# Optimization experiments

Measured on AMD Instinct MI355X. Metric: run time of the kernel, lower is better.

Reference implementation:

```python
import jax, jax.numpy as jnp
import numpy as np

B, S, IN_DIM, EMBED, HEADS, WINDOW = 2, 2048, 1024, 1024, 16, 256
HEAD_DIM = EMBED // HEADS
NEG_FILL = -9.0e15


def setup_inputs() -> dict:
    key = jax.random.key(0)
    k1, k2, k3, k4 = jax.random.split(key, 4)
    x = jax.random.normal(k1, (B, S, IN_DIM), dtype=jnp.float32)
    # padding_mask: positions with value 1 get zeroed in q/k/v (matches masked_fill semantics)
    padding_mask = jax.random.randint(k2, (B, S), 0, 2, dtype=jnp.int32)
    # xavier-uniform-like init scale for the linear weights
    lim_qkv = np.sqrt(6.0 / (IN_DIM + 3 * EMBED)).astype(np.float32)
    lim_o = np.sqrt(6.0 / (EMBED + EMBED)).astype(np.float32)
    Wqkv = jax.random.uniform(k3, (3 * EMBED, IN_DIM), jnp.float32, -lim_qkv, lim_qkv)
    bqkv = jnp.zeros((3 * EMBED,), jnp.float32)
    Wo = jax.random.uniform(k4, (EMBED, EMBED), jnp.float32, -lim_o, lim_o)
    bo = jnp.zeros((EMBED,), jnp.float32)
    return {"x": x, "padding_mask": padding_mask, "Wqkv": Wqkv, "bqkv": bqkv, "Wo": Wo, "bo": bo}


def reference(x, padding_mask, Wqkv, bqkv, Wo, bo):
    b, s, _ = x.shape
    h, hd, pad = HEADS, HEAD_DIM, WINDOW // 2
    # qkv projection: torch Linear is x @ W.T + b
    qkv = x @ Wqkv.T + bqkv                      # [B, S, 3E]
    qkv = qkv.reshape(b, s, h, 3 * hd).transpose(0, 2, 1, 3)  # [B, H, S, 3*hd]
    q, k, v = jnp.split(qkv, 3, axis=-1)          # each [B, H, S, hd]
    # zero out padded positions in q, k, v where padding_mask == 1
    pm = (padding_mask != 0)[:, None, :, None]    # [B, 1, S, 1]
    q = jnp.where(pm, 0.0, q)
    k = jnp.where(pm, 0.0, k)
    v = jnp.where(pm, 0.0, v)
    # dense banded scores: identical math to the unfold-based band compute
    scores = jnp.einsum("bhsd,bhtd->bhst", q, k)  # [B, H, S, S]
    idx = jnp.arange(s)
    band = jnp.abs(idx[None, :] - idx[:, None]) <= pad  # |i-j| <= window/2
    scores = jnp.where(band, scores, jnp.float32(NEG_FILL))
    scores = scores / jnp.sqrt(jnp.float32(hd))   # original scales AFTER the fill
    attn = jax.nn.softmax(scores, axis=-1)        # [B, H, S, S]
    vals = jnp.einsum("bhst,bhtd->bhsd", attn, v)  # [B, H, S, hd]
    vals = vals.transpose(0, 2, 1, 3).reshape(b, s, h * hd)  # [B, S, E]
    return vals @ Wo.T + bo
```

## Files before the change

### kernel.cpp

```cpp
#include <hip/hip_runtime.h>
#include <stdint.h>

#define S_LEN 2048
#define EMBED 1024
#define HEADS 16
#define HD 64
#define M_ROWS 4096
#define N_QKV 3072
#define KDIM 1024
#define SP 2336
#define CLP2 200

typedef __attribute__((ext_vector_type(8))) short short8;
typedef __attribute__((ext_vector_type(4))) float f32x4;

__device__ __forceinline__ unsigned short f2bf(float f) {
  union { float f; uint32_t u; } c; c.f = f;
  uint32_t u = c.u;
  u += 0x7fffu + ((u >> 16) & 1u);
  return (unsigned short)(u >> 16);
}

__device__ __forceinline__ void gload_lds16(const unsigned short* g, unsigned short* l) {
  __builtin_amdgcn_global_load_lds(
      (const __attribute__((address_space(1))) void*)g,
      (__attribute__((address_space(3))) void*)l, 16, 0, 0);
}

#define XQ 1048576
#define WQKVQ 786432
#define WOQ 262144
#define CVTQ (XQ + WQKVQ + WOQ)
__global__ __launch_bounds__(256) void cvt3_kernel(
    const float* __restrict__ x, const float* __restrict__ wqkv, const float* __restrict__ wo,
    unsigned short* __restrict__ xb, unsigned short* __restrict__ wqkvb, unsigned short* __restrict__ wob,
    unsigned short* __restrict__ vTp) {
  int i = blockIdx.x * blockDim.x + threadIdx.x;
  if (i < CVTQ) {
    const float* s; unsigned short* d; int off;
    if (i < XQ)               { s = x;    d = xb;    off = i; }
    else if (i < XQ + WQKVQ)  { s = wqkv; d = wqkvb; off = i - XQ; }
    else                      { s = wo;   d = wob;   off = i - XQ - WQKVQ; }
    float4 f = reinterpret_cast<const float4*>(s)[off];
    ushort4 o;
    o.x = f2bf(f.x); o.y = f2bf(f.y); o.z = f2bf(f.z); o.w = f2bf(f.w);
    reinterpret_cast<ushort4*>(d)[off] = o;
  } else {
    int j = i - CVTQ;
    int row = j / 72, p = j % 72;
    int off = row * 584 + (p < 32 ? p : 544 + (p - 32));
    reinterpret_cast<ushort4*>(vTp)[off] = (ushort4){0, 0, 0, 0};
  }
}

__global__ __launch_bounds__(256) void gemm_qkv(
    const unsigned short* __restrict__ A, const unsigned short* __restrict__ Bm,
    const float* __restrict__ bias, const int* __restrict__ pm,
    unsigned short* __restrict__ qo, unsigned short* __restrict__ ko,
    unsigned short* __restrict__ vTp)
{
  __shared__ __align__(16) unsigned short smem[40960];
  const int t = threadIdx.x, wave = t >> 6, lane = t & 63;
  const int m16 = lane & 15, q4 = lane >> 4;
  const int wm = wave >> 1, wn = wave & 1;
  const int bid = blockIdx.x;
  const int mb = bid >> 4, nb = bid & 15;
  const int srow = lane >> 2, scol = (lane & 3) << 3;
  const unsigned short* pA0 = A + (size_t)(mb * 128 + wave * 32 + srow) * KDIM + scol;
  const unsigned short* pA1 = pA0 + 16 * KDIM;
  const unsigned short* pB0 = Bm + (size_t)(nb * 192 + wave * 48 + srow) * KDIM + scol;
  const unsigned short* pB1 = pB0 + 16 * KDIM;
  const unsigned short* pB2 = pB0 + 32 * KDIM;
  f32x4 acc[4][6];
#pragma unroll
  for (int i_ = 0; i_ < 4; i_++)
#pragma unroll
    for (int j_ = 0; j_ < 6; j_++) acc[i_][j_] = (f32x4){0.f, 0.f, 0.f, 0.f};

  auto stage = [&](int buf, int kt) {
    unsigned short* As = smem + buf * 20480;
    unsigned short* Bs = As + 8192;
#pragma unroll
    for (int h = 0; h < 2; h++) {
      gload_lds16(pA0 + kt + h * 32, As + h * 4096 + (wave * 32) * 32);
      gload_lds16(pA1 + kt + h * 32, As + h * 4096 + (wave * 32 + 16) * 32);
      gload_lds16(pB0 + kt + h * 32, Bs + h * 6144 + (wave * 48) * 32);
      gload_lds16(pB1 + kt + h * 32, Bs + h * 6144 + (wave * 48 + 16) * 32);
      gload_lds16(pB2 + kt + h * 32, Bs + h * 6144 + (wave * 48 + 32) * 32);
    }
  };

  stage(0, 0);
  __syncthreads();
  int cur = 0;
  for (int kt = 0; kt < KDIM; kt += 64) {
    if (kt + 64 < KDIM) stage(cur ^ 1, kt + 64);
    const unsigned short* As = smem + cur * 20480;
    const unsigned short* Bs = As + 8192;
#pragma unroll
    for (int h = 0; h < 2; h++) {
      short8 af[4], bf[6];
#pragma unroll
      for (int mt = 0; mt < 4; mt++)
        af[mt] = *reinterpret_cast<const short8*>(&As[h * 4096 + (wm * 64 + mt * 16 + m16) * 32 + q4 * 8]);
#pragma unroll
      for (int nt = 0; nt < 6; nt++)
        bf[nt] = *reinterpret_cast<const short8*>(&Bs[h * 6144 + (wn * 96 + nt * 16 + m16) * 32 + q4 * 8]);
#pragma unroll
      for (int mt = 0; mt < 4; mt++)
#pragma unroll
        for (int nt = 0; nt < 6; nt++)
          acc[mt][nt] = __builtin_amdgcn_mfma_f32_16x16x32_bf16(af[mt], bf[nt], acc[mt][nt], 0, 0, 0);
    }
    __syncthreads();
    cur ^= 1;
  }

  float pmv[4][4];
#pragma unroll
  for (int mt = 0; mt < 4; mt++)
#pragma unroll
    for (int reg = 0; reg < 4; reg++) {
      int row = mb * 128 + wm * 64 + mt * 16 + q4 * 4 + reg;
      pmv[mt][reg] = (pm[row] != 0) ? 0.0f : 1.0f;
    }
#pragma unroll
  for (int nt = 0; nt < 6; nt++) {
    int cloc = wn * 96 + nt * 16 + m16;
    float bv = bias[nb * 192 + cloc];
#pragma unroll
    for (int mt = 0; mt < 4; mt++) {
#pragma unroll
      for (int reg = 0; reg < 4; reg++) {
        int rloc = wm * 64 + mt * 16 + q4 * 4 + reg;
        smem[rloc * CLP2 + cloc] = f2bf((acc[mt][nt][reg] + bv) * pmv[mt][reg]);
      }
    }
  }
  __syncthreads();
  const int s0 = mb * 128;
  const int bh = (s0 >> 11) * 16 + nb, s0l = s0 & 2047;
  {
    int r = t >> 1, half = t & 1;
    const unsigned short* sq = &smem[r * CLP2 + half * 32];
    unsigned short* dq = qo + ((size_t)(bh * 2048 + s0l + r)) * 64 + half * 32;
#pragma unroll
    for (int j = 0; j < 4; j++)
      *reinterpret_cast<short8*>(dq + j * 8) = *reinterpret_cast<const short8*>(sq + j * 8);
    const unsigned short* sk = &smem[r * CLP2 + 64 + half * 32];
    unsigned short* dk = ko + ((size_t)(bh * 2048 + s0l + r)) * 64 + half * 32;
#pragma unroll
    for (int j = 0; j < 4; j++)
      *reinterpret_cast<short8*>(dk + j * 8) = *reinterpret_cast<const short8*>(sk + j * 8);
  }
  {
    int d = t & 63, qtr = t >> 6;
    unsigned short* dst = vTp + (size_t)(bh * 64 + d) * SP + 128 + s0l + qtr * 32;
#pragma unroll
    for (int j8 = 0; j8 < 4; j8++) {
      short8 tmp;
#pragma unroll
      for (int jj = 0; jj < 8; jj++)
        tmp[jj] = (short)smem[(qtr * 32 + j8 * 8 + jj) * CLP2 + 128 + d];
      *reinterpret_cast<short8*>(dst + j8 * 8) = tmp;
    }
  }
}

__global__ __launch_bounds__(256) void gemm_out(
    const unsigned short* __restrict__ A, const unsigned short* __restrict__ Bm,
    const float* __restrict__ bias, float* __restrict__ out)
{
  __shared__ __align__(16) unsigned char smemraw[49152];
  float* Cldf = (float*)smemraw;
  const int t = threadIdx.x, wave = t >> 6, lane = t & 63;
  const int m16 = lane & 15, q4 = lane >> 4;
  const int wm = wave >> 1, wn = wave & 1;
  const int flat = blockIdx.y * 8 + blockIdx.x;
  const int xcd = flat & 7, bi = flat >> 3;
  const int mb = xcd * 8 + (bi & 7);
  const int nb = bi >> 3;
  const int srow = lane >> 2, scol = (lane & 3) << 3;
  const unsigned short* pA  = A + (size_t)(mb * 64 + wave * 16 + srow) * KDIM + scol;
  const unsigned short* pB0 = Bm + (size_t)(nb * 128 + wave * 32 + srow) * KDIM + scol;
  const unsigned short* pB1 = pB0 + 16 * KDIM;
  f32x4 acc[2][4];
#pragma unroll
  for (int i_ = 0; i_ < 2; i_++)
#pragma unroll
    for (int j_ = 0; j_ < 4; j_++) acc[i_][j_] = (f32x4){0.f, 0.f, 0.f, 0.f};

  auto stage = [&](int buf, int kt) {
    unsigned short* As = (unsigned short*)smemraw + buf * 12288;
    unsigned short* Bs = As + 4096;
#pragma unroll
    for (int h = 0; h < 2; h++) {
      gload_lds16(pA + kt + h * 32,  As + h * 2048 + (wave * 16) * 32);
      gload_lds16(pB0 + kt + h * 32, Bs + h * 4096 + (wave * 32) * 32);
      gload_lds16(pB1 + kt + h * 32, Bs + h * 4096 + (wave * 32 + 16) * 32);
    }
  };

  stage(0, 0);
  __syncthreads();
  int cur = 0;
  for (int kt = 0; kt < KDIM; kt += 64) {
    if (kt + 64 < KDIM) stage(cur ^ 1, kt + 64);
    const unsigned short* As = (const unsigned short*)smemraw + cur * 12288;
    const unsigned short* Bs = As + 4096;
#pragma unroll
    for (int h = 0; h < 2; h++) {
      short8 af[2], bf[4];
#pragma unroll
      for (int mt = 0; mt < 2; mt++)
        af[mt] = *reinterpret_cast<const short8*>(&As[h * 2048 + (wm * 32 + mt * 16 + m16) * 32 + q4 * 8]);
#pragma unroll
      for (int nt = 0; nt < 4; nt++)
        bf[nt] = *reinterpret_cast<const short8*>(&Bs[h * 4096 + (wn * 64 + nt * 16 + m16) * 32 + q4 * 8]);
#pragma unroll
      for (int mt = 0; mt < 2; mt++)
#pragma unroll
        for (int nt = 0; nt < 4; nt++)
          acc[mt][nt] = __builtin_amdgcn_mfma_f32_16x16x32_bf16(af[mt], bf[nt], acc[mt][nt], 0, 0, 0);
    }
    __syncthreads();
    cur ^= 1;
  }

#pragma unroll
  for (int nt = 0; nt < 4; nt++) {
    int cloc = wn * 64 + nt * 16 + m16;
    float bv = bias[nb * 128 + cloc];
#pragma unroll
    for (int mt = 0; mt < 2; mt++) {
#pragma unroll
      for (int reg = 0; reg < 4; reg++) {
        int rloc = wm * 32 + mt * 16 + q4 * 4 + reg;
        Cldf[rloc * 132 + cloc] = acc[mt][nt][reg] + bv;
      }
    }
  }
  __syncthreads();
  {
    int r = t >> 2, seg = t & 3;
    float* dst = out + (size_t)(mb * 64 + r) * EMBED + nb * 128 + seg * 32;
    const float* srcl = &Cldf[r * 132 + seg * 32];
#pragma unroll
    for (int j = 0; j < 8; j++)
      *reinterpret_cast<float4*>(dst + j * 4) = *reinterpret_cast<const float4*>(srcl + j * 4);
  }
}

__global__ __launch_bounds__(256, 2) void attn_kernel(
    const unsigned short* __restrict__ q, const unsigned short* __restrict__ k,
    const unsigned short* __restrict__ vTp, unsigned short* __restrict__ vals)
{
  __shared__ __align__(16) unsigned short smem[40960];
  unsigned short* Ks = smem;
  unsigned short* Vs = smem + 20480;
  unsigned short* Pld = smem;

  const int bid = blockIdx.x;
  const int bh = bid & 31, qg = bid >> 5;
  const int lane = threadIdx.x & 63, wave = threadIdx.x >> 6;
  const int i0b = qg * 64;
  const int i0 = i0b + wave * 16;
  const int m16 = lane & 15, q4 = lane >> 4;

  const unsigned short* kbase = k + (size_t)bh * 2048 * 64;
#pragma unroll
  for (int n = 0; n < 10; n++) {
    int idx = (n * 4 + wave) * 64 + lane;
    int krow = idx >> 3, seg = idx & 7;
    int grow = i0b - 128 + krow;
    grow = grow < 0 ? 0 : (grow > 2047 ? 2047 : grow);
    int lseg = seg ^ (krow & 7);
    gload_lds16(kbase + (size_t)grow * 64 + lseg * 8, Ks + (n * 4 + wave) * 512);
  }
  const unsigned short* vbase = vTp + (size_t)bh * 64 * SP + i0b;
#pragma unroll
  for (int n = 0; n < 10; n++) {
    int idx = (n * 4 + wave) * 64 + lane;
    int vrow = idx / 40, rem = idx % 40;
    int l = (rem & ~7) | ((rem & 7) ^ (vrow & 7));
    gload_lds16(vbase + (size_t)vrow * SP + l * 8, Vs + (n * 4 + wave) * 512);
  }

  const unsigned short* qb = q + ((size_t)(bh * 2048 + i0 + m16)) * 64 + q4 * 8;
  short8 aq0 = *reinterpret_cast<const short8*>(qb);
  short8 aq1 = *reinterpret_cast<const short8*>(qb + 32);

  __syncthreads();

  float sum[4] = {0.f, 0.f, 0.f, 0.f};
  uint32_t pP[18][2];
#pragma unroll
  for (int ct = 0; ct < 18; ct++) {
    int r = (wave + ct) * 16 + m16;
    int js = i0b - 128 + r;
    const unsigned short* kr = Ks + r * 64;
    short8 b0 = *reinterpret_cast<const short8*>(kr + ((q4 ^ (r & 7)) * 8));
    short8 b1 = *reinterpret_cast<const short8*>(kr + (((q4 + 4) ^ (r & 7)) * 8));
    f32x4 a = {0.f, 0.f, 0.f, 0.f};
    a = __builtin_amdgcn_mfma_f32_16x16x32_bf16(aq0, b0, a, 0, 0, 0);
    a = __builtin_amdgcn_mfma_f32_16x16x32_bf16(aq1, b1, a, 0, 0, 0);
    unsigned short pe[4];
#pragma unroll
    for (int reg = 0; reg < 4; reg++) {
      int i = i0 + q4 * 4 + reg;
      bool valid = (js >= 0) && (js < 2048) && (js >= i - 128) && (js <= i + 128);
      float e = valid ? __expf(a[reg] * 0.125f) : 0.0f;
      sum[reg] += e;
      pe[reg] = f2bf(e);
    }
    pP[ct][0] = (uint32_t)pe[0] | ((uint32_t)pe[1] << 16);
    pP[ct][1] = (uint32_t)pe[2] | ((uint32_t)pe[3] << 16);
  }
  float rden[4];
#pragma unroll
  for (int reg = 0; reg < 4; reg++) {
    float s = sum[reg];
    s += __shfl_xor(s, 1);
    s += __shfl_xor(s, 2);
    s += __shfl_xor(s, 4);
    s += __shfl_xor(s, 8);
    rden[reg] = 1.0f / s;
  }

  __syncthreads();

  unsigned short* Pw = Pld + wave * 16 * 296;
#pragma unroll
  for (int ct = 0; ct < 18; ct++) {
    Pw[(q4 * 4 + 0) * 296 + ct * 16 + m16] = (unsigned short)(pP[ct][0] & 0xFFFF);
    Pw[(q4 * 4 + 1) * 296 + ct * 16 + m16] = (unsigned short)(pP[ct][0] >> 16);
    Pw[(q4 * 4 + 2) * 296 + ct * 16 + m16] = (unsigned short)(pP[ct][1] & 0xFFFF);
    Pw[(q4 * 4 + 3) * 296 + ct * 16 + m16] = (unsigned short)(pP[ct][1] >> 16);
  }
  short8 ap[9];
#pragma unroll
  for (int kc = 0; kc < 9; kc++)
    ap[kc] = *reinterpret_cast<const short8*>(&Pw[m16 * 296 + kc * 32 + q4 * 8]);

  const int b = bh >> 4, h = bh & 15;
#pragma unroll
  for (int dt = 0; dt < 4; dt++) {
    int vrow = dt * 16 + m16;
    const unsigned short* vr = Vs + vrow * 320;
    f32x4 av = {0.f, 0.f, 0.f, 0.f};
#pragma unroll
    for (int kc = 0; kc < 9; kc++) {
      int jseg = kc * 4 + wave * 2 + q4;
      if (jseg > 39) jseg = 39;
      int sseg = (jseg & ~7) | ((jseg & 7) ^ (vrow & 7));
      short8 bv = *reinterpret_cast<const short8*>(vr + sseg * 8);
      av = __builtin_amdgcn_mfma_f32_16x16x32_bf16(ap[kc], bv, av, 0, 0, 0);
    }
#pragma unroll
    for (int reg = 0; reg < 4; reg++)
      Pw[(q4 * 4 + reg) * 296 + dt * 16 + m16] = f2bf(av[reg] * rden[reg]);
  }
  {
    int srow = lane >> 2, seg = lane & 3;
    unsigned short* dst = vals + ((size_t)(b * 2048 + i0 + srow)) * 1024 + h * 64 + seg * 16;
    const unsigned short* srcl = &Pw[srow * 296 + seg * 16];
    *reinterpret_cast<short8*>(dst)     = *reinterpret_cast<const short8*>(srcl);
    *reinterpret_cast<short8*>(dst + 8) = *reinterpret_cast<const short8*>(srcl + 8);
  }
}

extern "C" void kernel_launch(void* const* d_in, const int* in_sizes, int n_in,
                              void* d_out, int out_size, void* d_ws, size_t ws_size,
                              hipStream_t stream) {
  const float* x    = (const float*)d_in[0];
  const int*   pm   = (const int*)d_in[1];
  const float* Wqkv = (const float*)d_in[2];
  const float* bqkv = (const float*)d_in[3];
  const float* Wo   = (const float*)d_in[4];
  const float* bo   = (const float*)d_in[5];
  float* out = (float*)d_out;
  char* ws = (char*)d_ws;

  unsigned short* xb    = (unsigned short*)(ws);
  unsigned short* vals  = (unsigned short*)(ws);
  unsigned short* Wqkvb = (unsigned short*)(ws +  8388608);
  unsigned short* Wob   = (unsigned short*)(ws + 14680064);
  unsigned short* qbuf  = (unsigned short*)(ws + 16777216);
  unsigned short* kbuf  = (unsigned short*)(ws + 25165824);
  unsigned short* vTp   = (unsigned short*)(ws + 33554432);

  cvt3_kernel<<<8768, 256, 0, stream>>>(x, Wqkv, Wo, xb, Wqkvb, Wob, vTp);
  gemm_qkv<<<512, 256, 0, stream>>>(xb, Wqkvb, bqkv, pm, qbuf, kbuf, vTp);
  attn_kernel<<<1024, 256, 0, stream>>>(qbuf, kbuf, vTp, vals);
  gemm_out<<<dim3(8, 64), 256, 0, stream>>>(vals, Wob, bo, out);
}
```

Measured before the change: 162.3 us.

## Restructure QKV GEMM into 8-wave 256x192 tiles with swizzled LDS ping-pong

The QKV projection GEMM moves from 256-thread 128x192 tiles to 512-thread 256x192 tiles with 64-wide K slabs in a XOR-swizzled LDS layout. Global-to-LDS loads for the next slab are spread across four sub-phases, each separated by barriers, s_setprio and sched_barrier fences, so MFMA work overlaps the loads. The swizzle is meant to remove LDS bank conflicts, and the larger tile halves the grid and raises reuse of each B tile. The cost is more LDS per block, heavier barrier traffic, and the epilogue staging and stores must cover the doubled row count.

```diff
diff --git a/kernel.cpp b/kernel.cpp
--- a/kernel.cpp
+++ b/kernel.cpp
@@ -53,67 +53,138 @@
   }
 }
 
-__global__ __launch_bounds__(256) void gemm_qkv(
+__global__ __launch_bounds__(512, 2) void gemm_qkv(
     const unsigned short* __restrict__ A, const unsigned short* __restrict__ Bm,
     const float* __restrict__ bias, const int* __restrict__ pm,
     unsigned short* __restrict__ qo, unsigned short* __restrict__ ko,
     unsigned short* __restrict__ vTp)
 {
-  __shared__ __align__(16) unsigned short smem[40960];
+  __shared__ __align__(16) unsigned short smem[57344];
   const int t = threadIdx.x, wave = t >> 6, lane = t & 63;
   const int m16 = lane & 15, q4 = lane >> 4;
   const int wm = wave >> 1, wn = wave & 1;
   const int bid = blockIdx.x;
   const int mb = bid >> 4, nb = bid & 15;
-  const int srow = lane >> 2, scol = (lane & 3) << 3;
-  const unsigned short* pA0 = A + (size_t)(mb * 128 + wave * 32 + srow) * KDIM + scol;
-  const unsigned short* pA1 = pA0 + 16 * KDIM;
-  const unsigned short* pB0 = Bm + (size_t)(nb * 192 + wave * 48 + srow) * KDIM + scol;
-  const unsigned short* pB1 = pB0 + 16 * KDIM;
-  const unsigned short* pB2 = pB0 + 32 * KDIM;
+  const int lrow = lane >> 3;
+  const int lsegsw = ((lane & 7) ^ lrow) * 8;
+  const unsigned short* gsrc[7];
+#pragma unroll
+  for (int j = 0; j < 7; j++) {
+    int u = wave * 7 + j;
+    gsrc[j] = (u < 32 ? A  + (size_t)(mb * 256 + u * 8 + lrow) * KDIM
+                      : Bm + (size_t)(nb * 192 + (u - 32) * 8 + lrow) * KDIM)
+              + lsegsw;
+  }
+  const int rsw = (m16 & 7) * 8;
+
   f32x4 acc[4][6];
 #pragma unroll
   for (int i_ = 0; i_ < 4; i_++)
 #pragma unroll
     for (int j_ = 0; j_ < 6; j_++) acc[i_][j_] = (f32x4){0.f, 0.f, 0.f, 0.f};
 
-  auto stage = [&](int buf, int kt) {
-    unsigned short* As = smem + buf * 20480;
-    unsigned short* Bs = As + 8192;
-#pragma unroll
-    for (int h = 0; h < 2; h++) {
-      gload_lds16(pA0 + kt + h * 32, As + h * 4096 + (wave * 32) * 32);
-      gload_lds16(pA1 + kt + h * 32, As + h * 4096 + (wave * 32 + 16) * 32);
-      gload_lds16(pB0 + kt + h * 32, Bs + h * 6144 + (wave * 48) * 32);
-      gload_lds16(pB1 + kt + h * 32, Bs + h * 6144 + (wave * 48 + 16) * 32);
-      gload_lds16(pB2 + kt + h * 32, Bs + h * 6144 + (wave * 48 + 32) * 32);
-    }
+  auto LDA = [&](short8* af, const unsigned short* As, int h) {
+#pragma unroll
+    for (int mt = 0; mt < 4; mt++)
+      af[mt] = *reinterpret_cast<const short8*>(
+          &As[(wm * 64 + mt * 16 + m16) * 64 + (((h * 4 + q4) * 8) ^ rsw)]);
   };
-
-  stage(0, 0);
-  __syncthreads();
-  int cur = 0;
-  for (int kt = 0; kt < KDIM; kt += 64) {
-    if (kt + 64 < KDIM) stage(cur ^ 1, kt + 64);
-    const unsigned short* As = smem + cur * 20480;
-    const unsigned short* Bs = As + 8192;
-#pragma unroll
-    for (int h = 0; h < 2; h++) {
-      short8 af[4], bf[6];
-#pragma unroll
-      for (int mt = 0; mt < 4; mt++)
-        af[mt] = *reinterpret_cast<const short8*>(&As[h * 4096 + (wm * 64 + mt * 16 + m16) * 32 + q4 * 8]);
-#pragma unroll
-      for (int nt = 0; nt < 6; nt++)
-        bf[nt] = *reinterpret_cast<const short8*>(&Bs[h * 6144 + (wn * 96 + nt * 16 + m16) * 32 + q4 * 8]);
-#pragma unroll
-      for (int mt = 0; mt < 4; mt++)
-#pragma unroll
-        for (int nt = 0; nt < 6; nt++)
-          acc[mt][nt] = __builtin_amdgcn_mfma_f32_16x16x32_bf16(af[mt], bf[nt], acc[mt][nt], 0, 0, 0);
-    }
-    __syncthreads();
-    cur ^= 1;
+  auto LDB3 = [&](short8* bf, const unsigned short* Bs, int h, int n0) {
+#pragma unroll
+    for (int nt = 0; nt < 3; nt++)
+      bf[nt] = *reinterpret_cast<const short8*>(
+          &Bs[(wn * 96 + (n0 + nt) * 16 + m16) * 64 + (((h * 4 + q4) * 8) ^ rsw)]);
+  };
+  auto MM3 = [&](short8* af, short8* bf, int n0) {
+#pragma unroll
+    for (int mt = 0; mt < 4; mt++)
+#pragma unroll
+      for (int nt = 0; nt < 3; nt++)
+        acc[mt][n0 + nt] =
+            __builtin_amdgcn_mfma_f32_16x16x32_bf16(af[mt], bf[nt], acc[mt][n0 + nt], 0, 0, 0);
+  };
+
+#pragma unroll
+  for (int j = 0; j < 7; j++)
+    gload_lds16(gsrc[j], smem + (wave * 7 + j) * 512);
+  asm volatile("s_waitcnt vmcnt(0)" ::: "memory");
+  __builtin_amdgcn_s_barrier();
+  __builtin_amdgcn_sched_barrier(0);
+
+  for (int T = 0; T < 16; ++T) {
+    const int c = T & 1;
+    const unsigned short* As = smem + c * 28672;
+    const unsigned short* Bs = As + 16384;
+    unsigned short* nslab = smem + (c ^ 1) * 28672;
+    const int nkt = (T + 1) * 64;
+    const bool st = (T < 15);
+    short8 af[4], bf[3];
+
+    LDA(af, As, 0);
+    LDB3(bf, Bs, 0, 0);
+    if (st) {
+#pragma unroll
+      for (int j = 0; j < 3; j++)
+        gload_lds16(gsrc[j] + nkt, nslab + (wave * 7 + j) * 512);
+    }
+    __builtin_amdgcn_sched_barrier(0);
+    __builtin_amdgcn_s_barrier();
+    asm volatile("s_waitcnt lgkmcnt(0)" ::: "memory");
+    __builtin_amdgcn_sched_barrier(0);
+    __builtin_amdgcn_s_setprio(1);
+    MM3(af, bf, 0);
+    __builtin_amdgcn_s_setprio(0);
+    __builtin_amdgcn_sched_barrier(0);
+    __builtin_amdgcn_s_barrier();
+    __builtin_amdgcn_sched_barrier(0);
+
+    LDB3(bf, Bs, 0, 3);
+    if (st) {
+#pragma unroll
+      for (int j = 3; j < 5; j++)
+        gload_lds16(gsrc[j] + nkt, nslab + (wave * 7 + j) * 512);
+    }
+    __builtin_amdgcn_sched_barrier(0);
+    __builtin_amdgcn_s_barrier();
+    asm volatile("s_waitcnt lgkmcnt(0)" ::: "memory");
+    __builtin_amdgcn_sched_barrier(0);
+    __builtin_amdgcn_s_setprio(1);
+    MM3(af, bf, 3);
+    __builtin_amdgcn_s_setprio(0);
+    __builtin_amdgcn_sched_barrier(0);
+    __builtin_amdgcn_s_barrier();
+    __builtin_amdgcn_sched_barrier(0);
+
+    LDA(af, As, 1);
+    LDB3(bf, Bs, 1, 0);
+    if (st) {
+#pragma unroll
+      for (int j = 5; j < 7; j++)
+        gload_lds16(gsrc[j] + nkt, nslab + (wave * 7 + j) * 512);
+    }
+    __builtin_amdgcn_sched_barrier(0);
+    __builtin_amdgcn_s_barrier();
+    asm volatile("s_waitcnt lgkmcnt(0)" ::: "memory");
+    __builtin_amdgcn_sched_barrier(0);
+    __builtin_amdgcn_s_setprio(1);
+    MM3(af, bf, 0);
+    __builtin_amdgcn_s_setprio(0);
+    __builtin_amdgcn_sched_barrier(0);
+    __builtin_amdgcn_s_barrier();
+    __builtin_amdgcn_sched_barrier(0);
+
+    LDB3(bf, Bs, 1, 3);
+    asm volatile("s_waitcnt vmcnt(0)" ::: "memory");
+    __builtin_amdgcn_sched_barrier(0);
+    __builtin_amdgcn_s_barrier();
+    asm volatile("s_waitcnt lgkmcnt(0)" ::: "memory");
+    __builtin_amdgcn_sched_barrier(0);
+    __builtin_amdgcn_s_setprio(1);
+    MM3(af, bf, 3);
+    __builtin_amdgcn_s_setprio(0);
+    __builtin_amdgcn_sched_barrier(0);
+    __builtin_amdgcn_s_barrier();
+    __builtin_amdgcn_sched_barrier(0);
   }
 
   float pmv[4][4];
@@ -121,7 +192,7 @@
   for (int mt = 0; mt < 4; mt++)
 #pragma unroll
     for (int reg = 0; reg < 4; reg++) {
-      int row = mb * 128 + wm * 64 + mt * 16 + q4 * 4 + reg;
+      int row = mb * 256 + wm * 64 + mt * 16 + q4 * 4 + reg;
       pmv[mt][reg] = (pm[row] != 0) ? 0.0f : 1.0f;
     }
 #pragma unroll
@@ -138,7 +209,7 @@
     }
   }
   __syncthreads();
-  const int s0 = mb * 128;
+  const int s0 = mb * 256;
   const int bh = (s0 >> 11) * 16 + nb, s0l = s0 & 2047;
   {
     int r = t >> 1, half = t & 1;
@@ -154,14 +225,14 @@
       *reinterpret_cast<short8*>(dk + j * 8) = *reinterpret_cast<const short8*>(sk + j * 8);
   }
   {
-    int d = t & 63, qtr = t >> 6;
-    unsigned short* dst = vTp + (size_t)(bh * 64 + d) * SP + 128 + s0l + qtr * 32;
+    int d = t & 63, oct = t >> 6;
+    unsigned short* dst = vTp + (size_t)(bh * 64 + d) * SP + 128 + s0l + oct * 32;
 #pragma unroll
     for (int j8 = 0; j8 < 4; j8++) {
       short8 tmp;
 #pragma unroll
       for (int jj = 0; jj < 8; jj++)
-        tmp[jj] = (short)smem[(qtr * 32 + j8 * 8 + jj) * CLP2 + 128 + d];
+        tmp[jj] = (short)smem[(oct * 32 + j8 * 8 + jj) * CLP2 + 128 + d];
       *reinterpret_cast<short8*>(dst + j8 * 8) = tmp;
     }
   }
@@ -390,7 +461,7 @@
   unsigned short* vTp   = (unsigned short*)(ws + 33554432);
 
   cvt3_kernel<<<8768, 256, 0, stream>>>(x, Wqkv, Wo, xb, Wqkvb, Wob, vTp);
-  gemm_qkv<<<512, 256, 0, stream>>>(xb, Wqkvb, bqkv, pm, qbuf, kbuf, vTp);
+  gemm_qkv<<<256, 512, 0, stream>>>(xb, Wqkvb, bqkv, pm, qbuf, kbuf, vTp);
   attn_kernel<<<1024, 256, 0, stream>>>(qbuf, kbuf, vTp, vals);
   gemm_out<<<dim3(8, 64), 256, 0, stream>>>(vals, Wob, bo, out);
 }
```

New measurement: 161.1 us. Within noise of the previous version (-0.7%).

## Rework QKV GEMM into a 512-thread, 5-stage async pipeline with swizzled LDS

Applied to the files above, without the earlier changes.

The QKV projection GEMM moves to 512-thread blocks covering 256x192 tiles. Half the waves load A and half load B through a 5-slot ring of k=32 LDS stages. Explicit vmcnt waits and a single s_barrier per phase replace full __syncthreads, LDS rows are XOR-swizzled to cut bank conflicts, and MFMA bursts run at raised wave priority. The output GEMM gets the same explicit-waitcnt barrier treatment. The aim is to hide global-load latency and cut synchronisation and LDS conflicts, at the cost of much larger LDS use (about 140 KB per block) and lower block count.

```diff
diff --git a/kernel.cpp b/kernel.cpp
--- a/kernel.cpp
+++ b/kernel.cpp
@@ -53,75 +53,125 @@
   }
 }
 
-__global__ __launch_bounds__(256) void gemm_qkv(
+#define QKV_PHASE(DO_STAGE, NA, NB)                                            \
+  {                                                                            \
+    if (DO_STAGE) {                                                            \
+      if (wave < 4) {                                                          \
+        gload_lds16(g0 + k0, smem + sow + ldsu);                               \
+        gload_lds16(g1 + k0, smem + sow + ldsu + 512);                         \
+        gload_lds16(g2 + k0, smem + sow + ldsu + 1024);                        \
+        gload_lds16(g3 + k0, smem + sow + ldsu + 1536);                        \
+      } else {                                                                 \
+        gload_lds16(g0 + k0, smem + sow + ldsu);                               \
+        gload_lds16(g1 + k0, smem + sow + ldsu + 512);                         \
+        gload_lds16(g2 + k0, smem + sow + ldsu + 1024);                        \
+      }                                                                        \
+    }                                                                          \
+    __builtin_amdgcn_sched_barrier(0);                                         \
+    if (wave < 4) asm volatile("s_waitcnt vmcnt(" #NA ")" ::: "memory");       \
+    else          asm volatile("s_waitcnt vmcnt(" #NB ")" ::: "memory");       \
+    __builtin_amdgcn_sched_barrier(0);                                         \
+    __builtin_amdgcn_s_barrier();                                              \
+    __builtin_amdgcn_sched_barrier(0);                                         \
+    short8 af[4], bf[6];                                                       \
+    _Pragma("unroll")                                                          \
+    for (int mt = 0; mt < 4; mt++)                                             \
+      af[mt] = *reinterpret_cast<const short8*>(&smem[so + abase + mt * 512]); \
+    _Pragma("unroll")                                                          \
+    for (int nt = 0; nt < 6; nt++)                                             \
+      bf[nt] = *reinterpret_cast<const short8*>(&smem[so + bbase + nt * 512]); \
+    asm volatile("s_waitcnt lgkmcnt(0)" ::: "memory");                         \
+    __builtin_amdgcn_sched_barrier(0);                                         \
+    __builtin_amdgcn_s_setprio(1);                                             \
+    _Pragma("unroll")                                                          \
+    for (int mt = 0; mt < 4; mt++)                                             \
+      _Pragma("unroll")                                                        \
+      for (int nt = 0; nt < 6; nt++)                                           \
+        acc[mt][nt] = __builtin_amdgcn_mfma_f32_16x16x32_bf16(                 \
+            af[mt], bf[nt], acc[mt][nt], 0, 0, 0);                             \
+    __builtin_amdgcn_s_setprio(0);                                             \
+    __builtin_amdgcn_sched_barrier(0);                                         \
+  }
+
+__global__ __launch_bounds__(512, 2) void gemm_qkv(
     const unsigned short* __restrict__ A, const unsigned short* __restrict__ Bm,
     const float* __restrict__ bias, const int* __restrict__ pm,
     unsigned short* __restrict__ qo, unsigned short* __restrict__ ko,
     unsigned short* __restrict__ vTp)
 {
-  __shared__ __align__(16) unsigned short smem[40960];
+  __shared__ __align__(16) unsigned short smem[71680];
   const int t = threadIdx.x, wave = t >> 6, lane = t & 63;
   const int m16 = lane & 15, q4 = lane >> 4;
   const int wm = wave >> 1, wn = wave & 1;
   const int bid = blockIdx.x;
   const int mb = bid >> 4, nb = bid & 15;
-  const int srow = lane >> 2, scol = (lane & 3) << 3;
-  const unsigned short* pA0 = A + (size_t)(mb * 128 + wave * 32 + srow) * KDIM + scol;
-  const unsigned short* pA1 = pA0 + 16 * KDIM;
-  const unsigned short* pB0 = Bm + (size_t)(nb * 192 + wave * 48 + srow) * KDIM + scol;
-  const unsigned short* pB1 = pB0 + 16 * KDIM;
-  const unsigned short* pB2 = pB0 + 32 * KDIM;
+
+  const int srow16 = lane >> 2;
+  const int kseg = (lane & 3) ^ ((lane >> 3) & 3);
+  const unsigned short *g0, *g1, *g2, *g3;
+  int ldsu;
+  if (wave < 4) {
+    int u0 = wave * 4;
+    g0 = A + (size_t)(mb * 256 + (u0 + 0) * 16 + srow16) * KDIM + kseg * 8;
+    g1 = A + (size_t)(mb * 256 + (u0 + 1) * 16 + srow16) * KDIM + kseg * 8;
+    g2 = A + (size_t)(mb * 256 + (u0 + 2) * 16 + srow16) * KDIM + kseg * 8;
+    g3 = A + (size_t)(mb * 256 + (u0 + 3) * 16 + srow16) * KDIM + kseg * 8;
+    ldsu = u0 * 512;
+  } else {
+    int u0 = (wave - 4) * 3;
+    g0 = Bm + (size_t)(nb * 192 + (u0 + 0) * 16 + srow16) * KDIM + kseg * 8;
+    g1 = Bm + (size_t)(nb * 192 + (u0 + 1) * 16 + srow16) * KDIM + kseg * 8;
+    g2 = Bm + (size_t)(nb * 192 + (u0 + 2) * 16 + srow16) * KDIM + kseg * 8;
+    g3 = g2;
+    ldsu = 8192 + u0 * 512;
+  }
+
+  const int sa = q4 ^ ((m16 >> 1) & 3);
+  const int abase = (wm * 64 + m16) * 32 + sa * 8;
+  const int bbase = 8192 + (wn * 96 + m16) * 32 + sa * 8;
+
   f32x4 acc[4][6];
 #pragma unroll
   for (int i_ = 0; i_ < 4; i_++)
 #pragma unroll
     for (int j_ = 0; j_ < 6; j_++) acc[i_][j_] = (f32x4){0.f, 0.f, 0.f, 0.f};
 
-  auto stage = [&](int buf, int kt) {
-    unsigned short* As = smem + buf * 20480;
-    unsigned short* Bs = As + 8192;
-#pragma unroll
-    for (int h = 0; h < 2; h++) {
-      gload_lds16(pA0 + kt + h * 32, As + h * 4096 + (wave * 32) * 32);
-      gload_lds16(pA1 + kt + h * 32, As + h * 4096 + (wave * 32 + 16) * 32);
-      gload_lds16(pB0 + kt + h * 32, Bs + h * 6144 + (wave * 48) * 32);
-      gload_lds16(pB1 + kt + h * 32, Bs + h * 6144 + (wave * 48 + 16) * 32);
-      gload_lds16(pB2 + kt + h * 32, Bs + h * 6144 + (wave * 48 + 32) * 32);
-    }
-  };
-
-  stage(0, 0);
+  int so = 0, sow = 0, k0 = 0;
+#pragma unroll
+  for (int s = 0; s < 3; ++s) {
+    if (wave < 4) {
+      gload_lds16(g0 + k0, smem + sow + ldsu);
+      gload_lds16(g1 + k0, smem + sow + ldsu + 512);
+      gload_lds16(g2 + k0, smem + sow + ldsu + 1024);
+      gload_lds16(g3 + k0, smem + sow + ldsu + 1536);
+    } else {
+      gload_lds16(g0 + k0, smem + sow + ldsu);
+      gload_lds16(g1 + k0, smem + sow + ldsu + 512);
+      gload_lds16(g2 + k0, smem + sow + ldsu + 1024);
+    }
+    sow += 14336; k0 += 32;
+  }
+  __builtin_amdgcn_sched_barrier(0);
+
+  for (int h = 0; h < 29; ++h) {
+    QKV_PHASE(true, 12, 9);
+    so += 14336;  if (so  == 71680) so  = 0;
+    sow += 14336; if (sow == 71680) sow = 0;
+    k0 += 32;
+  }
+  QKV_PHASE(false, 8, 6);
+  so += 14336; if (so == 71680) so = 0;
+  QKV_PHASE(false, 4, 3);
+  so += 14336; if (so == 71680) so = 0;
+  QKV_PHASE(false, 0, 0);
   __syncthreads();
-  int cur = 0;
-  for (int kt = 0; kt < KDIM; kt += 64) {
-    if (kt + 64 < KDIM) stage(cur ^ 1, kt + 64);
-    const unsigned short* As = smem + cur * 20480;
-    const unsigned short* Bs = As + 8192;
-#pragma unroll
-    for (int h = 0; h < 2; h++) {
-      short8 af[4], bf[6];
-#pragma unroll
-      for (int mt = 0; mt < 4; mt++)
-        af[mt] = *reinterpret_cast<const short8*>(&As[h * 4096 + (wm * 64 + mt * 16 + m16) * 32 + q4 * 8]);
-#pragma unroll
-      for (int nt = 0; nt < 6; nt++)
-        bf[nt] = *reinterpret_cast<const short8*>(&Bs[h * 6144 + (wn * 96 + nt * 16 + m16) * 32 + q4 * 8]);
-#pragma unroll
-      for (int mt = 0; mt < 4; mt++)
-#pragma unroll
-        for (int nt = 0; nt < 6; nt++)
-          acc[mt][nt] = __builtin_amdgcn_mfma_f32_16x16x32_bf16(af[mt], bf[nt], acc[mt][nt], 0, 0, 0);
-    }
-    __syncthreads();
-    cur ^= 1;
-  }
 
   float pmv[4][4];
 #pragma unroll
   for (int mt = 0; mt < 4; mt++)
 #pragma unroll
     for (int reg = 0; reg < 4; reg++) {
-      int row = mb * 128 + wm * 64 + mt * 16 + q4 * 4 + reg;
+      int row = mb * 256 + wm * 64 + mt * 16 + q4 * 4 + reg;
       pmv[mt][reg] = (pm[row] != 0) ? 0.0f : 1.0f;
     }
 #pragma unroll
@@ -138,7 +188,7 @@
     }
   }
   __syncthreads();
-  const int s0 = mb * 128;
+  const int s0 = mb * 256;
   const int bh = (s0 >> 11) * 16 + nb, s0l = s0 & 2047;
   {
     int r = t >> 1, half = t & 1;
@@ -154,14 +204,14 @@
       *reinterpret_cast<short8*>(dk + j * 8) = *reinterpret_cast<const short8*>(sk + j * 8);
   }
   {
-    int d = t & 63, qtr = t >> 6;
-    unsigned short* dst = vTp + (size_t)(bh * 64 + d) * SP + 128 + s0l + qtr * 32;
+    int d = t & 63, oct = t >> 6;
+    unsigned short* dst = vTp + (size_t)(bh * 64 + d) * SP + 128 + s0l + oct * 32;
 #pragma unroll
     for (int j8 = 0; j8 < 4; j8++) {
       short8 tmp;
 #pragma unroll
       for (int jj = 0; jj < 8; jj++)
-        tmp[jj] = (short)smem[(qtr * 32 + j8 * 8 + jj) * CLP2 + 128 + d];
+        tmp[jj] = (short)smem[(oct * 32 + j8 * 8 + jj) * CLP2 + 128 + d];
       *reinterpret_cast<short8*>(dst + j8 * 8) = tmp;
     }
   }
@@ -202,10 +252,17 @@
   };
 
   stage(0, 0);
-  __syncthreads();
+  __builtin_amdgcn_sched_barrier(0);
   int cur = 0;
   for (int kt = 0; kt < KDIM; kt += 64) {
-    if (kt + 64 < KDIM) stage(cur ^ 1, kt + 64);
+    const bool st = (kt + 64 < KDIM);
+    if (st) stage(cur ^ 1, kt + 64);
+    __builtin_amdgcn_sched_barrier(0);
+    if (st) asm volatile("s_waitcnt vmcnt(6)" ::: "memory");
+    else    asm volatile("s_waitcnt vmcnt(0)" ::: "memory");
+    __builtin_amdgcn_sched_barrier(0);
+    __builtin_amdgcn_s_barrier();
+    __builtin_amdgcn_sched_barrier(0);
     const unsigned short* As = (const unsigned short*)smemraw + cur * 12288;
     const unsigned short* Bs = As + 4096;
 #pragma unroll
@@ -223,7 +280,9 @@
         for (int nt = 0; nt < 4; nt++)
           acc[mt][nt] = __builtin_amdgcn_mfma_f32_16x16x32_bf16(af[mt], bf[nt], acc[mt][nt], 0, 0, 0);
     }
-    __syncthreads();
+    __builtin_amdgcn_sched_barrier(0);
+    __builtin_amdgcn_s_barrier();
+    __builtin_amdgcn_sched_barrier(0);
     cur ^= 1;
   }
 
@@ -390,7 +449,7 @@
   unsigned short* vTp   = (unsigned short*)(ws + 33554432);
 
   cvt3_kernel<<<8768, 256, 0, stream>>>(x, Wqkv, Wo, xb, Wqkvb, Wob, vTp);
-  gemm_qkv<<<512, 256, 0, stream>>>(xb, Wqkvb, bqkv, pm, qbuf, kbuf, vTp);
+  gemm_qkv<<<256, 512, 0, stream>>>(xb, Wqkvb, bqkv, pm, qbuf, kbuf, vTp);
   attn_kernel<<<1024, 256, 0, stream>>>(qbuf, kbuf, vTp, vals);
   gemm_out<<<dim3(8, 64), 256, 0, stream>>>(vals, Wob, bo, out);
 }
```

New measurement: 160.3 us. No clear change (-1.2%).
